# Optimization experiments

Hardware: AMD Instinct MI355X
Metric: run time of the kernel (lower is better)

Reference implementation:

```python
import jax, jax.numpy as jnp
import numpy as np

DIM = 512
N_HEADS = 8
HEAD_DIM = DIM // N_HEADS
KERNEL = 31
HALF_K = KERNEL // 2  # 15
EPS = 1e-5


def setup_inputs() -> dict:
    key = jax.random.key(0)
    ks = jax.random.split(key, 6)
    B, L, D = 2, 2048, DIM
    x = jax.random.normal(ks[0], (B, L, D), dtype=jnp.float32)
    # torch nn.Linear(dim, 3*dim): y = x @ W.T + b; store transposed for x @ W
    Wqkv = jax.random.normal(ks[1], (D, 3 * D), dtype=jnp.float32) * (1.0 / np.sqrt(D))
    bqkv = jnp.zeros((3 * D,), dtype=jnp.float32)
    Wproj = jax.random.normal(ks[2], (D, D), dtype=jnp.float32) * (1.0 / np.sqrt(D))
    bproj = jnp.zeros((D,), dtype=jnp.float32)
    gamma = jnp.ones((D,), dtype=jnp.float32)
    beta = jnp.zeros((D,), dtype=jnp.float32)
    return {"x": x, "Wqkv": Wqkv, "bqkv": bqkv, "Wproj": Wproj,
            "bproj": bproj, "gamma": gamma, "beta": beta}


def reference(x, Wqkv, bqkv, Wproj, bproj, gamma, beta):
    B, L, D = x.shape
    residual = x
    qkv = x @ Wqkv + bqkv                                  # (B, L, 3D)
    qkv = qkv.reshape(B, L, 3, N_HEADS, HEAD_DIM)
    q = jnp.transpose(qkv[:, :, 0], (0, 2, 1, 3))          # (B, H, L, d)
    k = jnp.transpose(qkv[:, :, 1], (0, 2, 1, 3))
    v = jnp.transpose(qkv[:, :, 2], (0, 2, 1, 3))

    # sliding-window band mask: |i - j| <= half_k (dilation == 1)
    pos = jnp.arange(L)
    mask = jnp.abs(pos[None, :] - pos[:, None]) <= HALF_K  # (L, L)

    scale = HEAD_DIM ** -0.5
    attn = jnp.einsum('bhqd,bhkd->bhqk', q, k) * scale     # (B, H, L, L)
    attn = jnp.where(mask[None, None], attn, -jnp.inf)
    attn = jax.nn.softmax(attn, axis=-1)
    attn = jnp.nan_to_num(attn, nan=0.0)
    out = jnp.einsum('bhqk,bhkd->bhqd', attn, v)           # (B, H, L, d)
    out = jnp.transpose(out, (0, 2, 1, 3)).reshape(B, L, D)

    out = out @ Wproj + bproj                              # dropout: eval no-op
    y = out + residual
    mu = jnp.mean(y, axis=-1, keepdims=True)
    var = jnp.var(y, axis=-1, keepdims=True)
    return (y - mu) * jax.lax.rsqrt(var + EPS) * gamma + beta
```

## Files before the change

### kernel.cpp

```cpp
#include <hip/hip_runtime.h>

typedef unsigned short u16;
typedef unsigned int u32;
typedef __attribute__((ext_vector_type(8))) short bf16x8;
typedef __attribute__((ext_vector_type(4))) float f32x4;

#define DEV static __device__ __forceinline__

DEV u16 f2b(float x) {
  u32 u = __float_as_uint(x);
  u = (u + 0x7fffu + ((u >> 16) & 1u)) >> 16;
  return (u16)u;
}
DEV float b2f(u16 h) { return __uint_as_float(((u32)h) << 16); }

DEV f32x4 mfma16(bf16x8 a, bf16x8 b, f32x4 c) {
  return __builtin_amdgcn_mfma_f32_16x16x32_bf16(a, b, c, 0, 0, 0);
}

DEV void gload_lds16(const void* g, void* l) {
  __builtin_amdgcn_global_load_lds(
      (const __attribute__((address_space(1))) void*)g,
      (__attribute__((address_space(3))) void*)l, 16, 0, 0);
}

__global__ __launch_bounds__(256) void prep_kernel(
    const float* __restrict__ x, u16* __restrict__ xb,
    const float* __restrict__ Wqkv, u16* __restrict__ wqkvT,
    const float* __restrict__ Wproj, u16* __restrict__ wprojT) {
  __shared__ float tile[32][33];
  const int bid = blockIdx.x;
  const int tid = threadIdx.x;
  if (bid < 1024) {
    size_t i = (size_t)bid * 256 + tid;
    const f32x4 a = *(const f32x4*)(x + i * 8);
    const f32x4 b = *(const f32x4*)(x + i * 8 + 4);
    alignas(16) u16 t[8];
    t[0] = f2b(a[0]); t[1] = f2b(a[1]); t[2] = f2b(a[2]); t[3] = f2b(a[3]);
    t[4] = f2b(b[0]); t[5] = f2b(b[1]); t[6] = f2b(b[2]); t[7] = f2b(b[3]);
    *(bf16x8*)(xb + i * 8) = *(const bf16x8*)t;
    return;
  }
  const float* W;
  u16* WT;
  int C, bx, by;
  if (bid < 1024 + 768) {
    W = Wqkv; WT = wqkvT; C = 1536;
    bx = (bid - 1024) % 48; by = (bid - 1024) / 48;
  } else {
    W = Wproj; WT = wprojT; C = 512;
    bx = (bid - 1792) % 16; by = (bid - 1792) / 16;
  }
  int tx = tid & 31, ty = tid >> 5;
  int r0 = by * 32, c0 = bx * 32;
  for (int rr = ty; rr < 32; rr += 8)
    tile[rr][tx] = W[(size_t)(r0 + rr) * C + c0 + tx];
  __syncthreads();
  for (int rr = ty; rr < 32; rr += 8)
    WT[(size_t)(c0 + rr) * 512 + r0 + tx] = f2b(tile[tx][rr]);
}

template <int KDIM, int BM, int BN>
DEV void gemm_mainloop(const u16* __restrict__ A, const u16* __restrict__ Bt,
                       int m0, int n0, u16* __restrict__ As, u16* __restrict__ Bs,
                       f32x4 (&acc)[BM / 32][BN / 32]) {
  constexpr int MI = BM / 32, NI = BN / 32;
  constexpr int ACH = BM / 32, BCH = BN / 32;
  constexpr int LOADS = ACH + BCH;
  constexpr int NSTEP = KDIM / 64;
  const int tid = threadIdx.x;
  const int lane = tid & 63;
  const int wave = tid >> 6;
  const int rl = lane & 15;
  const int g = lane >> 4;
  const int wrow = (wave >> 1) * (BM / 2);
  const int wcol = (wave & 1) * (BN / 2);
  const f32x4 fz = {0.f, 0.f, 0.f, 0.f};
#pragma unroll
  for (int m = 0; m < MI; ++m)
#pragma unroll
    for (int n = 0; n < NI; ++n) acc[m][n] = fz;

  auto stage = [&](int k0, int buf) {
#pragma unroll
    for (int c = 0; c < ACH; ++c) {
      int f = c * 256 + tid;
      int row = f >> 3;
      int ko = (((f & 7) ^ (row & 7)) << 3);
      gload_lds16(A + (size_t)(m0 + row) * KDIM + k0 + ko,
                  (char*)As + buf * (BM * 128) + c * 4096 + wave * 1024);
    }
#pragma unroll
    for (int c = 0; c < BCH; ++c) {
      int f = c * 256 + tid;
      int row = f >> 3;
      int ko = (((f & 7) ^ (row & 7)) << 3);
      gload_lds16(Bt + (size_t)(n0 + row) * KDIM + k0 + ko,
                  (char*)Bs + buf * (BN * 128) + c * 4096 + wave * 1024);
    }
  };

  stage(0, 0);
  int buf = 0;
#pragma unroll
  for (int k = 0; k < NSTEP; ++k) {
    if (k + 1 < NSTEP) {
      stage((k + 1) * 64, buf ^ 1);
      asm volatile("s_waitcnt vmcnt(%0)" ::"i"(LOADS) : "memory");
    } else {
      asm volatile("s_waitcnt vmcnt(0)" ::: "memory");
    }
    __builtin_amdgcn_s_barrier();
    const u16* Ab = As + buf * (BM * 64);
    const u16* Bb = Bs + buf * (BN * 64);
    bf16x8 af[MI][2], bv[NI][2];
#pragma unroll
    for (int kk = 0; kk < 2; ++kk) {
      int sl = ((kk * 4 + g) ^ (rl & 7)) << 3;
#pragma unroll
      for (int m = 0; m < MI; ++m)
        af[m][kk] = *(const bf16x8*)(Ab + (size_t)(wrow + m * 16 + rl) * 64 + sl);
#pragma unroll
      for (int n = 0; n < NI; ++n)
        bv[n][kk] = *(const bf16x8*)(Bb + (size_t)(wcol + n * 16 + rl) * 64 + sl);
    }
    __builtin_amdgcn_s_setprio(1);
#pragma unroll
    for (int kk = 0; kk < 2; ++kk)
#pragma unroll
      for (int m = 0; m < MI; ++m)
#pragma unroll
        for (int n = 0; n < NI; ++n)
          acc[m][n] = mfma16(af[m][kk], bv[n][kk], acc[m][n]);
    __builtin_amdgcn_s_setprio(0);
    asm volatile("s_waitcnt lgkmcnt(0)" ::: "memory");
    __builtin_amdgcn_s_barrier();
    buf ^= 1;
  }
}

__global__ __launch_bounds__(256) void gemm_qkv_kernel(
    const u16* __restrict__ xb, const u16* __restrict__ wT, const float* __restrict__ bias,
    u16* __restrict__ qb, u16* __restrict__ kb, u16* __restrict__ vb) {
  __shared__ u16 As[2 * 64 * 64];
  __shared__ u16 Bs[2 * 128 * 64];
  f32x4 acc[2][4];
  int m0 = blockIdx.y * 64, n0 = blockIdx.x * 128;
  gemm_mainloop<512, 64, 128>(xb, wT, m0, n0, As, Bs, acc);
  const int lane = threadIdx.x & 63, wave = threadIdx.x >> 6;
  const int wrow = (wave >> 1) * 32, wcol = (wave & 1) * 64;
  const int g = lane >> 4, cl = lane & 15;
  for (int n = 0; n < 4; ++n) {
    int col = n0 + wcol + n * 16 + cl;
    int sid = col >> 9;
    int h = (col >> 6) & 7, d = col & 63;
    u16* dst = sid == 0 ? qb : (sid == 1 ? kb : vb);
    float bvv = bias[col];
    for (int m = 0; m < 2; ++m)
      for (int i = 0; i < 4; ++i) {
        int row = m0 + wrow + m * 16 + g * 4 + i;
        int bb = row >> 11, ll = row & 2047;
        dst[(((size_t)bb * 8 + h) * 2048 + ll) * 64 + d] = f2b(acc[m][n][i] + bvv);
      }
  }
}

__global__ __launch_bounds__(256) void attn_kernel(const u16* __restrict__ qb,
                                                   const u16* __restrict__ kb,
                                                   const u16* __restrict__ vb,
                                                   u16* __restrict__ ao) {
  __shared__ u16 Qs[64 * 72];
  __shared__ u16 Ks[96 * 72];
  __shared__ u16 Vt[64 * 104];
  __shared__ u16 Ps[64 * 104];
  const int tid = threadIdx.x;
  const int bh = blockIdx.y;
  const int q0 = blockIdx.x * 64;
  const int k0s = q0 - 16;
  const u16* qg = qb + ((size_t)bh * 2048 + q0) * 64;
  for (int c = tid; c < 512; c += 256) {
    int r = c >> 3, off = (c & 7) << 3;
    *(bf16x8*)&Qs[r * 72 + off] = *(const bf16x8*)&qg[r * 64 + off];
  }
  const bf16x8 z8 = {0, 0, 0, 0, 0, 0, 0, 0};
  for (int c = tid; c < 768; c += 256) {
    int r = c >> 3, off = (c & 7) << 3;
    int j = k0s + r;
    bf16x8 kv = z8, vv = z8;
    if (j >= 0 && j < 2048) {
      kv = *(const bf16x8*)&kb[((size_t)bh * 2048 + j) * 64 + off];
      vv = *(const bf16x8*)&vb[((size_t)bh * 2048 + j) * 64 + off];
    }
    *(bf16x8*)&Ks[r * 72 + off] = kv;
    const u16* vp = (const u16*)&vv;
    for (int jj = 0; jj < 8; ++jj) Vt[(size_t)(off + jj) * 104 + r] = vp[jj];
  }
  __syncthreads();

  const int w = tid >> 6, l = tid & 63, g = l >> 4, cl = l & 15;
  const f32x4 fz = {0.f, 0.f, 0.f, 0.f};
  f32x4 s[6];
  for (int n = 0; n < 6; ++n) s[n] = fz;
  for (int kk = 0; kk < 64; kk += 32) {
    bf16x8 a = *(const bf16x8*)&Qs[(size_t)(w * 16 + cl) * 72 + kk + g * 8];
    for (int n = 0; n < 6; ++n) {
      bf16x8 b = *(const bf16x8*)&Ks[(size_t)(n * 16 + cl) * 72 + kk + g * 8];
      s[n] = mfma16(a, b, s[n]);
    }
  }
  float pr[6][4];
  for (int i = 0; i < 4; ++i) {
    int qgl = q0 + w * 16 + g * 4 + i;
    float m = -1e30f;
    for (int n = 0; n < 6; ++n) {
      int jg = k0s + n * 16 + cl;
      bool valid = (jg >= 0) && (jg < 2048) && (jg >= qgl - 15) && (jg <= qgl + 15);
      float sv = valid ? s[n][i] * 0.125f : -1e30f;
      pr[n][i] = sv;
      m = fmaxf(m, sv);
    }
    m = fmaxf(m, __shfl_xor(m, 1));
    m = fmaxf(m, __shfl_xor(m, 2));
    m = fmaxf(m, __shfl_xor(m, 4));
    m = fmaxf(m, __shfl_xor(m, 8));
    float sm = 0.f;
    for (int n = 0; n < 6; ++n) {
      float e = __expf(pr[n][i] - m);
      pr[n][i] = e;
      sm += e;
    }
    sm += __shfl_xor(sm, 1);
    sm += __shfl_xor(sm, 2);
    sm += __shfl_xor(sm, 4);
    sm += __shfl_xor(sm, 8);
    float inv = 1.f / sm;
    for (int n = 0; n < 6; ++n)
      Ps[(size_t)(w * 16 + g * 4 + i) * 104 + n * 16 + cl] = f2b(pr[n][i] * inv);
  }
  __syncthreads();

  f32x4 o[4];
  for (int n = 0; n < 4; ++n) o[n] = fz;
  for (int ks = 0; ks < 96; ks += 32) {
    bf16x8 a = *(const bf16x8*)&Ps[(size_t)(w * 16 + cl) * 104 + ks + g * 8];
    for (int n = 0; n < 4; ++n) {
      bf16x8 b = *(const bf16x8*)&Vt[(size_t)(n * 16 + cl) * 104 + ks + g * 8];
      o[n] = mfma16(a, b, o[n]);
    }
  }
  int b_ = bh >> 3, h = bh & 7;
  for (int n = 0; n < 4; ++n)
    for (int i = 0; i < 4; ++i) {
      int qrow = q0 + w * 16 + g * 4 + i;
      ao[((size_t)b_ * 2048 + qrow) * 512 + h * 64 + n * 16 + cl] = f2b(o[n][i]);
    }
}

__global__ __launch_bounds__(256) void gemm_proj_kernel(
    const u16* __restrict__ ab, const u16* __restrict__ wT, const float* __restrict__ bias,
    const float* __restrict__ x, float* __restrict__ y) {
  __shared__ u16 As[2 * 64 * 64];
  __shared__ u16 Bs[2 * 64 * 64];
  f32x4 acc[2][2];
  int m0 = blockIdx.y * 64, n0 = blockIdx.x * 64;
  gemm_mainloop<512, 64, 64>(ab, wT, m0, n0, As, Bs, acc);
  const int lane = threadIdx.x & 63, wave = threadIdx.x >> 6;
  const int wrow = (wave >> 1) * 32, wcol = (wave & 1) * 32;
  const int g = lane >> 4, cl = lane & 15;
  for (int n = 0; n < 2; ++n) {
    int col = n0 + wcol + n * 16 + cl;
    float bvv = bias[col];
    for (int m = 0; m < 2; ++m)
      for (int i = 0; i < 4; ++i) {
        int row = m0 + wrow + m * 16 + g * 4 + i;
        size_t idx = (size_t)row * 512 + col;
        y[idx] = acc[m][n][i] + bvv + x[idx];
      }
  }
}

__global__ __launch_bounds__(256) void ln_kernel(const float* __restrict__ y,
                                                 const float* __restrict__ gamma,
                                                 const float* __restrict__ beta,
                                                 float* __restrict__ out) {
  int row = blockIdx.x * 4 + (threadIdx.x >> 6);
  int lane = threadIdx.x & 63;
  const float* yr = y + (size_t)row * 512 + lane * 8;
  alignas(16) float v[8];
  *(f32x4*)&v[0] = *(const f32x4*)yr;
  *(f32x4*)&v[4] = *(const f32x4*)(yr + 4);
  float sum = 0.f, sq = 0.f;
  for (int j = 0; j < 8; ++j) { sum += v[j]; sq += v[j] * v[j]; }
  for (int d = 1; d < 64; d <<= 1) {
    sum += __shfl_xor(sum, d);
    sq += __shfl_xor(sq, d);
  }
  float mean = sum * (1.f / 512.f);
  float var = sq * (1.f / 512.f) - mean * mean;
  float rstd = rsqrtf(var + 1e-5f);
  int c0 = lane * 8;
  alignas(16) float r[8];
  for (int j = 0; j < 8; ++j) r[j] = (v[j] - mean) * rstd * gamma[c0 + j] + beta[c0 + j];
  float* op = out + (size_t)row * 512 + c0;
  *(f32x4*)&op[0] = *(const f32x4*)&r[0];
  *(f32x4*)&op[4] = *(const f32x4*)&r[4];
}

extern "C" void kernel_launch(void* const* d_in, const int* in_sizes, int n_in,
                              void* d_out, int out_size, void* d_ws, size_t ws_size,
                              hipStream_t stream) {
  const float* x     = (const float*)d_in[0];
  const float* Wqkv  = (const float*)d_in[1];
  const float* bqkv  = (const float*)d_in[2];
  const float* Wproj = (const float*)d_in[3];
  const float* bproj = (const float*)d_in[4];
  const float* gamma = (const float*)d_in[5];
  const float* beta  = (const float*)d_in[6];
  float* out = (float*)d_out;
  char* ws = (char*)d_ws;

  u16* xb     = (u16*)(ws);
  u16* wqkvT  = (u16*)(ws + 4194304);
  u16* wprojT = (u16*)(ws + 5767168);
  u16* qb     = (u16*)(ws + 6291456);
  u16* kb     = (u16*)(ws + 10485760);
  u16* vb     = (u16*)(ws + 14680064);
  u16* ao     = (u16*)(ws + 18874368);
  float* y    = (float*)(ws + 23068672);

  prep_kernel<<<2048, 256, 0, stream>>>(x, xb, Wqkv, wqkvT, Wproj, wprojT);
  gemm_qkv_kernel<<<dim3(12, 64), 256, 0, stream>>>(xb, wqkvT, bqkv, qb, kb, vb);
  attn_kernel<<<dim3(32, 16), 256, 0, stream>>>(qb, kb, vb, ao);
  gemm_proj_kernel<<<dim3(8, 64), 256, 0, stream>>>(ao, wprojT, bproj, x, y);
  ln_kernel<<<1024, 256, 0, stream>>>(y, gamma, beta, out);
}
```

Before: 44.34 us.

## Stage GEMM and attention outputs through LDS for vectorized stores; swizzle V transpose

The QKV GEMM epilogue now writes its bias-added bf16 tile into shared memory, then issues 16-byte vectorized global stores to the head-split q/k/v layout instead of scattered 2-byte stores. The attention kernel stages its output tile through LDS the same way, and its transposed V buffer uses an XOR swizzle with a 128-element stride to reduce LDS bank conflicts on both the transpose writes and the MFMA operand reads. LayerNorm loads gamma and beta with vector loads. These changes add extra LDS traffic and barriers in exchange for coalesced global writes.

```diff
diff --git a/kernel.cpp b/kernel.cpp
--- a/kernel.cpp
+++ b/kernel.cpp
@@ -147,21 +147,29 @@
   f32x4 acc[2][4];
   int m0 = blockIdx.y * 64, n0 = blockIdx.x * 128;
   gemm_mainloop<512, 64, 128>(xb, wT, m0, n0, As, Bs, acc);
-  const int lane = threadIdx.x & 63, wave = threadIdx.x >> 6;
+  const int tid = threadIdx.x;
+  const int lane = tid & 63, wave = tid >> 6;
   const int wrow = (wave >> 1) * 32, wcol = (wave & 1) * 64;
   const int g = lane >> 4, cl = lane & 15;
+  u16* Cs = Bs;
   for (int n = 0; n < 4; ++n) {
-    int col = n0 + wcol + n * 16 + cl;
-    int sid = col >> 9;
-    int h = (col >> 6) & 7, d = col & 63;
+    int col = wcol + n * 16 + cl;
+    float bvv = bias[n0 + col];
+    for (int m = 0; m < 2; ++m)
+      for (int i = 0; i < 4; ++i)
+        Cs[(size_t)(wrow + m * 16 + g * 4 + i) * 136 + col] = f2b(acc[m][n][i] + bvv);
+  }
+  __syncthreads();
+  for (int it = 0; it < 4; ++it) {
+    int id = it * 256 + tid;
+    int r = id >> 4, ch = id & 15;
+    bf16x8 v = *(const bf16x8*)&Cs[(size_t)r * 136 + ch * 8];
+    int grow = m0 + r;
+    int gcol = n0 + ch * 8;
+    int sid = gcol >> 9, h = (gcol >> 6) & 7, d = gcol & 63;
     u16* dst = sid == 0 ? qb : (sid == 1 ? kb : vb);
-    float bvv = bias[col];
-    for (int m = 0; m < 2; ++m)
-      for (int i = 0; i < 4; ++i) {
-        int row = m0 + wrow + m * 16 + g * 4 + i;
-        int bb = row >> 11, ll = row & 2047;
-        dst[(((size_t)bb * 8 + h) * 2048 + ll) * 64 + d] = f2b(acc[m][n][i] + bvv);
-      }
+    int bb = grow >> 11, ll = grow & 2047;
+    *(bf16x8*)&dst[(((size_t)bb * 8 + h) * 2048 + ll) * 64 + d] = v;
   }
 }
 
@@ -171,7 +179,7 @@
                                                    u16* __restrict__ ao) {
   __shared__ u16 Qs[64 * 72];
   __shared__ u16 Ks[96 * 72];
-  __shared__ u16 Vt[64 * 104];
+  __shared__ u16 Vt[64 * 128];
   __shared__ u16 Ps[64 * 104];
   const int tid = threadIdx.x;
   const int bh = blockIdx.y;
@@ -193,7 +201,10 @@
     }
     *(bf16x8*)&Ks[r * 72 + off] = kv;
     const u16* vp = (const u16*)&vv;
-    for (int jj = 0; jj < 8; ++jj) Vt[(size_t)(off + jj) * 104 + r] = vp[jj];
+    for (int jj = 0; jj < 8; ++jj) {
+      int d = off + jj;
+      Vt[(size_t)d * 128 + (((r >> 3) ^ ((d >> 3) & 7)) << 3) + (r & 7)] = vp[jj];
+    }
   }
   __syncthreads();
 
@@ -244,16 +255,25 @@
   for (int ks = 0; ks < 96; ks += 32) {
     bf16x8 a = *(const bf16x8*)&Ps[(size_t)(w * 16 + cl) * 104 + ks + g * 8];
     for (int n = 0; n < 4; ++n) {
-      bf16x8 b = *(const bf16x8*)&Vt[(size_t)(n * 16 + cl) * 104 + ks + g * 8];
+      int d = n * 16 + cl;
+      int cc = ((ks >> 3) + g) ^ ((d >> 3) & 7);
+      bf16x8 b = *(const bf16x8*)&Vt[(size_t)d * 128 + (cc << 3)];
       o[n] = mfma16(a, b, o[n]);
     }
   }
+  __syncthreads();
+  u16* Os = Ps;
+  for (int n = 0; n < 4; ++n)
+    for (int i = 0; i < 4; ++i)
+      Os[(size_t)(w * 16 + g * 4 + i) * 72 + n * 16 + cl] = f2b(o[n][i]);
+  __syncthreads();
   int b_ = bh >> 3, h = bh & 7;
-  for (int n = 0; n < 4; ++n)
-    for (int i = 0; i < 4; ++i) {
-      int qrow = q0 + w * 16 + g * 4 + i;
-      ao[((size_t)b_ * 2048 + qrow) * 512 + h * 64 + n * 16 + cl] = f2b(o[n][i]);
-    }
+  for (int it = 0; it < 2; ++it) {
+    int id = it * 256 + tid;
+    int r = id >> 3, ch = id & 7;
+    bf16x8 v = *(const bf16x8*)&Os[(size_t)r * 72 + ch * 8];
+    *(bf16x8*)&ao[((size_t)b_ * 2048 + q0 + r) * 512 + h * 64 + ch * 8] = v;
+  }
 }
 
 __global__ __launch_bounds__(256) void gemm_proj_kernel(
@@ -299,8 +319,13 @@
   float var = sq * (1.f / 512.f) - mean * mean;
   float rstd = rsqrtf(var + 1e-5f);
   int c0 = lane * 8;
+  alignas(16) float gmv[8], btv[8];
+  *(f32x4*)&gmv[0] = *(const f32x4*)(gamma + c0);
+  *(f32x4*)&gmv[4] = *(const f32x4*)(gamma + c0 + 4);
+  *(f32x4*)&btv[0] = *(const f32x4*)(beta + c0);
+  *(f32x4*)&btv[4] = *(const f32x4*)(beta + c0 + 4);
   alignas(16) float r[8];
-  for (int j = 0; j < 8; ++j) r[j] = (v[j] - mean) * rstd * gamma[c0 + j] + beta[c0 + j];
+  for (int j = 0; j < 8; ++j) r[j] = (v[j] - mean) * rstd * gmv[j] + btv[j];
   float* op = out + (size_t)row * 512 + c0;
   *(f32x4*)&op[0] = *(const f32x4*)&r[0];
   *(f32x4*)&op[4] = *(const f32x4*)&r[4];
```

New measurement: 45.37 us. 2.3% more time.

## Fuse projection GEMM with LayerNorm via last-block flags; retile QKV GEMM; swizzle Vt

Applied to the files above, without the earlier changes.

Merges the LayerNorm pass into the projection GEMM. The last of the 8 column blocks for each 64-row stripe, found with an atomic counter, normalizes that stripe, which removes one kernel launch. The QKV GEMM tile width drops from 128 to 96 columns with an occupancy hint, giving more blocks, and the transposed V buffer in attention gets an XOR swizzle to cut LDS bank conflicts. The fused path relies on relaxed agent-scope atomics without an explicit fence, adds a memset launch, and leaves only 64 blocks doing the LayerNorm tail.

```diff
diff --git a/kernel.cpp b/kernel.cpp
--- a/kernel.cpp
+++ b/kernel.cpp
@@ -139,18 +139,18 @@
   }
 }
 
-__global__ __launch_bounds__(256) void gemm_qkv_kernel(
+__global__ __launch_bounds__(256, 4) void gemm_qkv_kernel(
     const u16* __restrict__ xb, const u16* __restrict__ wT, const float* __restrict__ bias,
     u16* __restrict__ qb, u16* __restrict__ kb, u16* __restrict__ vb) {
   __shared__ u16 As[2 * 64 * 64];
-  __shared__ u16 Bs[2 * 128 * 64];
-  f32x4 acc[2][4];
-  int m0 = blockIdx.y * 64, n0 = blockIdx.x * 128;
-  gemm_mainloop<512, 64, 128>(xb, wT, m0, n0, As, Bs, acc);
+  __shared__ u16 Bs[2 * 96 * 64];
+  f32x4 acc[2][3];
+  int m0 = blockIdx.y * 64, n0 = blockIdx.x * 96;
+  gemm_mainloop<512, 64, 96>(xb, wT, m0, n0, As, Bs, acc);
   const int lane = threadIdx.x & 63, wave = threadIdx.x >> 6;
-  const int wrow = (wave >> 1) * 32, wcol = (wave & 1) * 64;
+  const int wrow = (wave >> 1) * 32, wcol = (wave & 1) * 48;
   const int g = lane >> 4, cl = lane & 15;
-  for (int n = 0; n < 4; ++n) {
+  for (int n = 0; n < 3; ++n) {
     int col = n0 + wcol + n * 16 + cl;
     int sid = col >> 9;
     int h = (col >> 6) & 7, d = col & 63;
@@ -171,7 +171,7 @@
                                                    u16* __restrict__ ao) {
   __shared__ u16 Qs[64 * 72];
   __shared__ u16 Ks[96 * 72];
-  __shared__ u16 Vt[64 * 104];
+  __shared__ u16 Vt[64 * 128];
   __shared__ u16 Ps[64 * 104];
   const int tid = threadIdx.x;
   const int bh = blockIdx.y;
@@ -193,7 +193,10 @@
     }
     *(bf16x8*)&Ks[r * 72 + off] = kv;
     const u16* vp = (const u16*)&vv;
-    for (int jj = 0; jj < 8; ++jj) Vt[(size_t)(off + jj) * 104 + r] = vp[jj];
+    for (int jj = 0; jj < 8; ++jj) {
+      int d = off + jj;
+      Vt[(size_t)d * 128 + (((r >> 3) ^ ((d >> 3) & 7)) << 3) + (r & 7)] = vp[jj];
+    }
   }
   __syncthreads();
 
@@ -244,7 +247,9 @@
   for (int ks = 0; ks < 96; ks += 32) {
     bf16x8 a = *(const bf16x8*)&Ps[(size_t)(w * 16 + cl) * 104 + ks + g * 8];
     for (int n = 0; n < 4; ++n) {
-      bf16x8 b = *(const bf16x8*)&Vt[(size_t)(n * 16 + cl) * 104 + ks + g * 8];
+      int d = n * 16 + cl;
+      int cc = ((ks >> 3) + g) ^ ((d >> 3) & 7);
+      bf16x8 b = *(const bf16x8*)&Vt[(size_t)d * 128 + (cc << 3)];
       o[n] = mfma16(a, b, o[n]);
     }
   }
@@ -256,15 +261,19 @@
     }
 }
 
-__global__ __launch_bounds__(256) void gemm_proj_kernel(
+__global__ __launch_bounds__(256) void gemm_proj_ln_kernel(
     const u16* __restrict__ ab, const u16* __restrict__ wT, const float* __restrict__ bias,
-    const float* __restrict__ x, float* __restrict__ y) {
+    const float* __restrict__ x, float* __restrict__ y,
+    const float* __restrict__ gamma, const float* __restrict__ beta,
+    float* __restrict__ out, int* __restrict__ flags) {
   __shared__ u16 As[2 * 64 * 64];
   __shared__ u16 Bs[2 * 64 * 64];
+  __shared__ int lastFlag;
   f32x4 acc[2][2];
   int m0 = blockIdx.y * 64, n0 = blockIdx.x * 64;
   gemm_mainloop<512, 64, 64>(ab, wT, m0, n0, As, Bs, acc);
-  const int lane = threadIdx.x & 63, wave = threadIdx.x >> 6;
+  const int tid = threadIdx.x;
+  const int lane = tid & 63, wave = tid >> 6;
   const int wrow = (wave >> 1) * 32, wcol = (wave & 1) * 32;
   const int g = lane >> 4, cl = lane & 15;
   for (int n = 0; n < 2; ++n) {
@@ -274,36 +283,48 @@
       for (int i = 0; i < 4; ++i) {
         int row = m0 + wrow + m * 16 + g * 4 + i;
         size_t idx = (size_t)row * 512 + col;
-        y[idx] = acc[m][n][i] + bvv + x[idx];
+        float vv = acc[m][n][i] + bvv + x[idx];
+        __hip_atomic_store(&y[idx], vv, __ATOMIC_RELAXED, __HIP_MEMORY_SCOPE_AGENT);
       }
   }
-}
-
-__global__ __launch_bounds__(256) void ln_kernel(const float* __restrict__ y,
-                                                 const float* __restrict__ gamma,
-                                                 const float* __restrict__ beta,
-                                                 float* __restrict__ out) {
-  int row = blockIdx.x * 4 + (threadIdx.x >> 6);
-  int lane = threadIdx.x & 63;
-  const float* yr = y + (size_t)row * 512 + lane * 8;
-  alignas(16) float v[8];
-  *(f32x4*)&v[0] = *(const f32x4*)yr;
-  *(f32x4*)&v[4] = *(const f32x4*)(yr + 4);
-  float sum = 0.f, sq = 0.f;
-  for (int j = 0; j < 8; ++j) { sum += v[j]; sq += v[j] * v[j]; }
-  for (int d = 1; d < 64; d <<= 1) {
-    sum += __shfl_xor(sum, d);
-    sq += __shfl_xor(sq, d);
-  }
-  float mean = sum * (1.f / 512.f);
-  float var = sq * (1.f / 512.f) - mean * mean;
-  float rstd = rsqrtf(var + 1e-5f);
-  int c0 = lane * 8;
-  alignas(16) float r[8];
-  for (int j = 0; j < 8; ++j) r[j] = (v[j] - mean) * rstd * gamma[c0 + j] + beta[c0 + j];
-  float* op = out + (size_t)row * 512 + c0;
-  *(f32x4*)&op[0] = *(const f32x4*)&r[0];
-  *(f32x4*)&op[4] = *(const f32x4*)&r[4];
+  __syncthreads();
+  if (tid == 0) {
+    int old = atomicAdd(&flags[blockIdx.y], 1);
+    lastFlag = (old == 7);
+  }
+  __syncthreads();
+  if (!lastFlag) return;
+
+  const int c0 = lane * 8;
+  alignas(16) float gmv[8], btv[8];
+  *(f32x4*)&gmv[0] = *(const f32x4*)(gamma + c0);
+  *(f32x4*)&gmv[4] = *(const f32x4*)(gamma + c0 + 4);
+  *(f32x4*)&btv[0] = *(const f32x4*)(beta + c0);
+  *(f32x4*)&btv[4] = *(const f32x4*)(beta + c0 + 4);
+  for (int rr = 0; rr < 16; ++rr) {
+    int row = m0 + wave * 16 + rr;
+    const float* yr = y + (size_t)row * 512 + c0;
+    float v[8];
+#pragma unroll
+    for (int j = 0; j < 8; ++j)
+      v[j] = __hip_atomic_load(yr + j, __ATOMIC_RELAXED, __HIP_MEMORY_SCOPE_AGENT);
+    float sum = 0.f, sq = 0.f;
+#pragma unroll
+    for (int j = 0; j < 8; ++j) { sum += v[j]; sq += v[j] * v[j]; }
+    for (int d = 1; d < 64; d <<= 1) {
+      sum += __shfl_xor(sum, d);
+      sq += __shfl_xor(sq, d);
+    }
+    float mean = sum * (1.f / 512.f);
+    float var = sq * (1.f / 512.f) - mean * mean;
+    float rstd = rsqrtf(var + 1e-5f);
+    alignas(16) float r[8];
+#pragma unroll
+    for (int j = 0; j < 8; ++j) r[j] = (v[j] - mean) * rstd * gmv[j] + btv[j];
+    float* op = out + (size_t)row * 512 + c0;
+    *(f32x4*)&op[0] = *(const f32x4*)&r[0];
+    *(f32x4*)&op[4] = *(const f32x4*)&r[4];
+  }
 }
 
 extern "C" void kernel_launch(void* const* d_in, const int* in_sizes, int n_in,
@@ -327,10 +348,12 @@
   u16* vb     = (u16*)(ws + 14680064);
   u16* ao     = (u16*)(ws + 18874368);
   float* y    = (float*)(ws + 23068672);
-
+  int* flags  = (int*)(ws + 31457280);
+
+  hipMemsetAsync(flags, 0, 64 * sizeof(int), stream);
   prep_kernel<<<2048, 256, 0, stream>>>(x, xb, Wqkv, wqkvT, Wproj, wprojT);
-  gemm_qkv_kernel<<<dim3(12, 64), 256, 0, stream>>>(xb, wqkvT, bqkv, qb, kb, vb);
+  gemm_qkv_kernel<<<dim3(16, 64), 256, 0, stream>>>(xb, wqkvT, bqkv, qb, kb, vb);
   attn_kernel<<<dim3(32, 16), 256, 0, stream>>>(qb, kb, vb, ao);
-  gemm_proj_kernel<<<dim3(8, 64), 256, 0, stream>>>(ao, wprojT, bproj, x, y);
-  ln_kernel<<<1024, 256, 0, stream>>>(y, gamma, beta, out);
-}
+  gemm_proj_ln_kernel<<<dim3(8, 64), 256, 0, stream>>>(ao, wprojT, bproj, x, y,
+                                                       gamma, beta, out, flags);
+}
```

After: 82.88 us. 1.87x slower.
